# Kernel optimization log

Hardware: AMD Instinct MI355X
Metric: run time of the kernel (lower is better)

The kernel has to match this reference:

```python
import jax, jax.numpy as jnp
import numpy as np

TEMP = 1.75   # temp_schedule(epoch=5, warmup=10): 2.5 - 1.5*0.5
ALPHA = 0.5   # blend_schedule(epoch=5): 0.2 + 0.6*0.5
EPS = 1e-5
HEADS = 2


def _ln(x, g, b):
    mu = x.mean(-1, keepdims=True)
    var = ((x - mu) ** 2).mean(-1, keepdims=True)
    return (x - mu) * jax.lax.rsqrt(var + EPS) * g + b


def _gelu(x):
    return jax.nn.gelu(x, approximate=False)  # torch nn.GELU default = exact erf


def _attn_pool(x, ln_g, ln_b, in_w, in_b, out_w, out_b):
    # x: [N, T, E]; nn.MultiheadAttention self-attention then mean over T
    N, T, E = x.shape
    Dh = E // HEADS
    xn = _ln(x, ln_g, ln_b)
    qkv = xn @ in_w + in_b                      # [N, T, 3E] (in_w stored [E, 3E])
    q, k, v = jnp.split(qkv, 3, axis=-1)
    q = q.reshape(N, T, HEADS, Dh).transpose(0, 2, 1, 3)
    k = k.reshape(N, T, HEADS, Dh).transpose(0, 2, 1, 3)
    v = v.reshape(N, T, HEADS, Dh).transpose(0, 2, 1, 3)
    scores = jnp.einsum('nhqd,nhkd->nhqk', q, k) / jnp.sqrt(jnp.float32(Dh))
    a = jax.nn.softmax(scores, axis=-1)
    o = jnp.einsum('nhqk,nhkd->nhqd', a, v).transpose(0, 2, 1, 3).reshape(N, T, E)
    o = o @ out_w + out_b                       # [N, T, E]
    return o.mean(axis=1)                       # [N, E]


def setup_inputs() -> dict:
    key = jax.random.key(0)
    ks = iter(jax.random.split(key, 40))
    B, L, T, D = 4, 24, 400, 1024
    H = D // 2  # 512
    G = 4       # groups
    s = 0.02
    r = lambda shp: jax.random.normal(next(ks), shp, dtype=jnp.float32) * s
    inp = {
        'x': jax.random.normal(next(ks), (B, L, T, D), dtype=jnp.float32),
        'mlp_alpha': jnp.ones((L,), jnp.float32),
        # shared MLP: LN -> Linear(D,H) -> GELU -> Linear(H,H)
        's_ln_g': jnp.ones((D,), jnp.float32), 's_ln_b': jnp.zeros((D,), jnp.float32),
        's_w1': r((D, H)), 's_b1': jnp.zeros((H,), jnp.float32),
        's_w2': r((H, H)), 's_b2': jnp.zeros((H,), jnp.float32),
        # 4 group MLPs (stacked)
        'g_ln_g': jnp.ones((G, D), jnp.float32), 'g_ln_b': jnp.zeros((G, D), jnp.float32),
        'g_w1': r((G, D, H)), 'g_b1': jnp.zeros((G, H), jnp.float32),
        'g_w2': r((G, H, H)), 'g_b2': jnp.zeros((G, H), jnp.float32),
        # TimeAttentionPool (shared module): LN + MHA(512, 2 heads) + out_proj
        'p_ln_g': jnp.ones((H,), jnp.float32), 'p_ln_b': jnp.zeros((H,), jnp.float32),
        'p_in_w': r((H, 3 * H)), 'p_in_b': jnp.zeros((3 * H,), jnp.float32),
        'p_out_w': r((H, H)), 'p_out_b': jnp.zeros((H,), jnp.float32),
        # router: Linear(512,128) -> GELU -> Linear(128,1) -> sigmoid(/temp)
        'r_w1': r((H, 128)), 'r_b1': jnp.zeros((128,), jnp.float32),
        'r_w2': r((128, 1)), 'r_b2': jnp.zeros((1,), jnp.float32),
        # post norms
        'pn_g': jnp.ones((H,), jnp.float32), 'pn_b': jnp.zeros((H,), jnp.float32),
        'pnf_g': jnp.ones((H,), jnp.float32), 'pnf_b': jnp.zeros((H,), jnp.float32),
        # classifier 512 -> 256 -> 128 -> 2
        'c_w1': r((H, H // 2)), 'c_b1': jnp.zeros((H // 2,), jnp.float32),
        'c_w2': r((H // 2, H // 4)), 'c_b2': jnp.zeros((H // 4,), jnp.float32),
        'c_w3': r((H // 4, 2)), 'c_b3': jnp.zeros((2,), jnp.float32),
    }
    return inp


def reference(x, mlp_alpha, s_ln_g, s_ln_b, s_w1, s_b1, s_w2, s_b2,
              g_ln_g, g_ln_b, g_w1, g_b1, g_w2, g_b2,
              p_ln_g, p_ln_b, p_in_w, p_in_b, p_out_w, p_out_b,
              r_w1, r_b1, r_w2, r_b2, pn_g, pn_b, pnf_g, pnf_b,
              c_w1, c_b1, c_w2, c_b2, c_w3, c_b3):
    B, L, T, D = x.shape
    G = g_w1.shape[0]
    S = L // G  # group_size = 6; expert i uses group i // S
    H = s_w1.shape[1]

    # shared MLP over all experts at once (dropout inactive in eval)
    xs = _ln(x, s_ln_g, s_ln_b)                              # [B,L,T,D]
    shared = _gelu(xs @ s_w1 + s_b1) @ s_w2 + s_b2           # [B,L,T,H]

    # group MLPs: experts i//S -> group; reshape L -> (G, S)
    xg = x.reshape(B, G, S, T, D)
    xgn = _ln(xg, g_ln_g[:, None, None, :], g_ln_b[:, None, None, :])
    hg = _gelu(jnp.einsum('bgstd,gdh->bgsth', xgn, g_w1) + g_b1[None, :, None, None, :])
    grp = jnp.einsum('bgsth,ghk->bgstk', hg, g_w2) + g_b2[None, :, None, None, :]
    grp = grp.reshape(B, L, T, H)

    weighted = shared + mlp_alpha[None, :, None, None] * grp  # [B,L,T,H]

    # attn-pool every expert stream (fold L into batch)
    time_pooled = _attn_pool(weighted.reshape(B * L, T, H),
                             p_ln_g, p_ln_b, p_in_w, p_in_b, p_out_w, p_out_b)
    time_pooled = time_pooled.reshape(B, L, H)               # [B,L,H]

    # router
    rh = _gelu(time_pooled @ r_w1 + r_b1)
    logits_r = (rh @ r_w2 + r_b2)[..., 0]                    # [B,L]
    learned = jax.nn.sigmoid(logits_r / TEMP)
    routing_weights = ALPHA * learned + (1.0 - ALPHA) / L

    # soft fusion over experts
    fusion = (weighted * routing_weights[:, :, None, None]).sum(axis=1)  # [B,T,H]
    fusion = _ln(fusion, pn_g, pn_b).mean(axis=1)            # [B,H]

    shared_mean = shared.mean(axis=1)                        # [B,T,H]
    time_ctx = _attn_pool(shared_mean, p_ln_g, p_ln_b, p_in_w, p_in_b, p_out_w, p_out_b)

    fused_all = _ln(fusion, pnf_g, pnf_b) + _ln(time_ctx, pnf_g, pnf_b)  # [B,H]

    h = _gelu(fused_all @ c_w1 + c_b1)
    h = _gelu(h @ c_w2 + c_b2)
    logits = h @ c_w3 + c_b3                                 # [B,2]
    return logits, routing_weights, fused_all, time_pooled
```

## Files before the change

### kernel.cpp

```cpp
#include <hip/hip_runtime.h>
#include <stdint.h>


typedef float f32x4 __attribute__((ext_vector_type(4)));
typedef short bf16x8 __attribute__((ext_vector_type(8)));

__device__ __forceinline__ float bf2f(unsigned short u) {
  return __uint_as_float(((unsigned int)u) << 16);
}
__device__ __forceinline__ unsigned short f2bf(float f) {
  unsigned int u = __float_as_uint(f);
  u += 0x7fffu + ((u >> 16) & 1u);
  return (unsigned short)(u >> 16);
}
__device__ __forceinline__ float gelu_f(float x) {
  return 0.5f * x * (1.0f + erff(x * 0.70710678118654752440f));
}

typedef __attribute__((address_space(1))) const unsigned int gas_u32;
typedef __attribute__((address_space(3))) unsigned int las_u32;
__device__ __forceinline__ void gload16(const unsigned short* g, unsigned short* l) {
  __builtin_amdgcn_global_load_lds((gas_u32*)g, (las_u32*)l, 16, 0, 0);
}

template <int EPI, int GROUPED>
__global__ __launch_bounds__(256) void gemm_bt(
    const unsigned short* __restrict__ A, const unsigned short* __restrict__ WT,
    const float* __restrict__ bias, unsigned short* __restrict__ Cout,
    const unsigned short* __restrict__ addbuf, const float* __restrict__ alpha_vec,
    unsigned short* __restrict__ vtbuf, int K, int N, int ldout, int Mslice) {
  const int tid = (int)threadIdx.x;
  const int w = tid >> 6, lane = tid & 63, g = lane >> 4, ql = lane & 15;
  const int z = blockIdx.z;
  const int wr = w >> 1, wc = w & 1;

  int bm, bn;
  if (!GROUPED) {
    const int nbm = (int)gridDim.x, nbn = (int)gridDim.y;
    const int nb = nbm * nbn;
    const int lin = (int)blockIdx.x + nbm * (int)blockIdx.y;
    const int q = nb >> 3, r8 = nb & 7;
    const int xcd = lin & 7, c = lin >> 3;
    const int base = (xcd < r8) ? xcd * (q + 1) : r8 * (q + 1) + (xcd - r8) * q;
    const int widx = base + c;
    bm = widx / nbn;
    bn = widx - bm * nbn;
  } else {
    bm = (int)blockIdx.x;
    bn = (int)blockIdx.y;
  }
  const int n0 = bn * 128;

  int rowbase, rows_here;
  const unsigned short* wt = WT;
  const float* bs = bias;
  float alpha = 0.f;
  if (GROUPED) {
    const int l_idx = z % 24;
    const int grp = l_idx / 6;
    rowbase = z * Mslice + bm * 128;
    rows_here = Mslice - bm * 128;
    if (rows_here > 128) rows_here = 128;
    wt = WT + (size_t)grp * (size_t)N * (size_t)K;
    bs = bias + (size_t)grp * (size_t)N;
    if (EPI == 2) alpha = alpha_vec[l_idx];
  } else {
    rowbase = bm * 128;
    rows_here = Mslice - bm * 128;
    if (rows_here > 128) rows_here = 128;
  }

  __shared__ __align__(16) unsigned short sA[2][128 * 32];
  __shared__ __align__(16) unsigned short sB[2][128 * 32];

  f32x4 acc[4][4];
#pragma unroll
  for (int i = 0; i < 4; ++i)
#pragma unroll
    for (int j = 0; j < 4; ++j) acc[i][j] = (f32x4){0.f, 0.f, 0.f, 0.f};

  const int swzg = (lane & 3) ^ ((lane >> 3) & 3);
  const int rA0 = w * 32 + (lane >> 2);
  const int rA1 = rA0 + 16;
  const int rA0c = rA0 < rows_here ? rA0 : rows_here - 1;
  const int rA1c = rA1 < rows_here ? rA1 : rows_here - 1;
  const unsigned short* a0p = A + (size_t)(rowbase + rA0c) * K + swzg * 8;
  const unsigned short* a1p = A + (size_t)(rowbase + rA1c) * K + swzg * 8;
  const unsigned short* b0p = wt + (size_t)(n0 + rA0) * K + swzg * 8;
  const unsigned short* b1p = wt + (size_t)(n0 + rA1) * K + swzg * 8;
  const int ldsw = w * 1024;

  const int aroff = (wr * 64 + ql) * 32 + ((g ^ ((ql >> 1) & 3)) * 8);
  const int broff = (wc * 64 + ql) * 32 + ((g ^ ((ql >> 1) & 3)) * 8);

  const int nsteps = K >> 5;
  gload16(a0p, &sA[0][ldsw]);
  gload16(a1p, &sA[0][ldsw + 512]);
  gload16(b0p, &sB[0][ldsw]);
  gload16(b1p, &sB[0][ldsw + 512]);
  __syncthreads();

  for (int s = 0; s < nsteps; ++s) {
    const int cur = s & 1;
    if (s + 1 < nsteps) {
      const int k0 = (s + 1) << 5;
      const int nxt = cur ^ 1;
      gload16(a0p + k0, &sA[nxt][ldsw]);
      gload16(a1p + k0, &sA[nxt][ldsw + 512]);
      gload16(b0p + k0, &sB[nxt][ldsw]);
      gload16(b1p + k0, &sB[nxt][ldsw + 512]);
    }
    bf16x8 af[4], bfr[4];
#pragma unroll
    for (int mi = 0; mi < 4; ++mi)
      af[mi] = *(const bf16x8*)(&sA[cur][aroff + mi * 512]);
#pragma unroll
    for (int ni = 0; ni < 4; ++ni)
      bfr[ni] = *(const bf16x8*)(&sB[cur][broff + ni * 512]);
#pragma unroll
    for (int mi = 0; mi < 4; ++mi)
#pragma unroll
      for (int ni = 0; ni < 4; ++ni)
        acc[mi][ni] =
            __builtin_amdgcn_mfma_f32_16x16x32_bf16(af[mi], bfr[ni], acc[mi][ni], 0, 0, 0);
    __syncthreads();
  }

#pragma unroll
  for (int mi = 0; mi < 4; ++mi) {
#pragma unroll
    for (int ni = 0; ni < 4; ++ni) {
      const int col = n0 + wc * 64 + ni * 16 + ql;
      const float bb = bs[col];
#pragma unroll
      for (int r = 0; r < 4; ++r) {
        const int rloc = wr * 64 + mi * 16 + 4 * g + r;
        if (rloc >= rows_here) continue;
        const int grow = rowbase + rloc;
        float v = acc[mi][ni][r] + bb;
        if (EPI == 1) v = gelu_f(v);
        if (EPI == 0 || EPI == 1) {
          Cout[(size_t)grow * ldout + col] = f2bf(v);
        } else if (EPI == 2) {
          const float sh = bf2f(addbuf[(size_t)grow * ldout + col]);
          Cout[(size_t)grow * ldout + col] = f2bf(sh + alpha * v);
        } else {
          if (col < 1024) {
            Cout[(size_t)grow * ldout + col] = f2bf(v);
          } else {
            vtbuf[(size_t)grow * 512 + (col - 1024)] = f2bf(v);
          }
        }
      }
    }
  }
}

__global__ void transpose_v(const unsigned short* __restrict__ vbuf,
                            unsigned short* __restrict__ vt) {
  const int p = blockIdx.z;
  const int h = p & 1, nst = p >> 1;
  const int t0 = blockIdx.x * 32, d0 = blockIdx.y * 32;
  __shared__ unsigned short tile[32][33];
  const int tx = threadIdx.x, ty = threadIdx.y;
#pragma unroll
  for (int i = 0; i < 4; ++i) {
    const int t = t0 + ty + i * 8;
    if (t < 400)
      tile[ty + i * 8][tx] = vbuf[((size_t)nst * 400 + t) * 512 + h * 256 + d0 + tx];
  }
  __syncthreads();
  const int t = t0 + tx;
  if (t < 400) {
#pragma unroll
    for (int i = 0; i < 4; ++i)
      vt[((size_t)p * 256 + d0 + ty + i * 8) * 400 + t] = tile[tx][ty + i * 8];
  }
}

__global__ __launch_bounds__(256, 2) void attn_fwd(const unsigned short* __restrict__ qk,
                                                   const unsigned short* __restrict__ vt,
                                                   unsigned short* __restrict__ outb) {
  const int nb = (int)gridDim.x;
  int flat = (int)blockIdx.x;
  flat = (flat & 7) * (nb >> 3) + (flat >> 3);
  const int qt = flat % 7;
  const int h = (flat / 7) & 1;
  const int n = flat / 14;
  const int q0 = qt * 64;

  const int tid = (int)threadIdx.x;
  const int w = tid >> 6, lane = tid & 63, g = lane >> 4, ql = lane & 15;

  __shared__ __align__(16) unsigned short slab[400 * 32];
  __shared__ __align__(16) unsigned short Pc[4][512];
  __shared__ float rs[4][16];

  const int qr = q0 + w * 16 + ql;
  const int qrc = qr < 400 ? qr : 399;
  const unsigned short* qp = qk + ((size_t)n * 400 + qrc) * 1024 + h * 256 + g * 8;
  bf16x8 qf[8];
#pragma unroll
  for (int d0 = 0; d0 < 8; ++d0) qf[d0] = *(const bf16x8*)(qp + d0 * 32);

  f32x4 st[25];
#pragma unroll
  for (int kf = 0; kf < 25; ++kf) st[kf] = (f32x4){0.f, 0.f, 0.f, 0.f};

  const unsigned short* kbase = qk + (size_t)n * 400 * 1024 + 512 + h * 256;
  for (int d0 = 0; d0 < 8; ++d0) {
    bf16x8 stg[7];
#pragma unroll
    for (int c = 0; c < 7; ++c) {
      const int q = tid + c * 256;
      const int r = q >> 2, slot = q & 3;
      if (r < 400)
        stg[c] = *(const bf16x8*)(kbase + (size_t)r * 1024 + d0 * 32 + slot * 8);
    }
    __syncthreads();
#pragma unroll
    for (int c = 0; c < 7; ++c) {
      const int q = tid + c * 256;
      const int r = q >> 2, slot = q & 3;
      if (r < 400) *(bf16x8*)(slab + r * 32 + (slot ^ ((r >> 1) & 3)) * 8) = stg[c];
    }
    __syncthreads();
#pragma unroll
    for (int kf = 0; kf < 25; ++kf) {
      const int r = kf * 16 + ql;
      bf16x8 kfr = *(const bf16x8*)(slab + r * 32 + ((g ^ ((r >> 1) & 3)) * 8));
      st[kf] = __builtin_amdgcn_mfma_f32_16x16x32_bf16(kfr, qf[d0], st[kf], 0, 0, 0);
    }
  }

  const float sc = 0.0625f;
  float m = -3.0e38f;
#pragma unroll
  for (int kf = 0; kf < 25; ++kf)
    m = fmaxf(m, fmaxf(fmaxf(st[kf][0], st[kf][1]), fmaxf(st[kf][2], st[kf][3])));
  m = fmaxf(m, __shfl_xor(m, 16));
  m = fmaxf(m, __shfl_xor(m, 32));
  float sum = 0.f;
  uint2 pp[25];
#pragma unroll
  for (int kf = 0; kf < 25; ++kf) {
    float e0 = expf((st[kf][0] - m) * sc);
    float e1 = expf((st[kf][1] - m) * sc);
    float e2 = expf((st[kf][2] - m) * sc);
    float e3 = expf((st[kf][3] - m) * sc);
    sum += (e0 + e1) + (e2 + e3);
    pp[kf].x = (unsigned int)f2bf(e0) | ((unsigned int)f2bf(e1) << 16);
    pp[kf].y = (unsigned int)f2bf(e2) | ((unsigned int)f2bf(e3) << 16);
  }
  sum += __shfl_xor(sum, 16);
  sum += __shfl_xor(sum, 32);
  if (g == 0) rs[w][ql] = sum;

  f32x4 oacc[16];
#pragma unroll
  for (int nf = 0; nf < 16; ++nf) oacc[nf] = (f32x4){0.f, 0.f, 0.f, 0.f};

  unsigned short* Pw = Pc[w];
  const unsigned short* vbase = vt + (size_t)(n * 2 + h) * 256 * 400;
  for (int kt = 0; kt < 13; ++kt) {
    const int k0 = kt * 32;
    bf16x8 stg[4];
#pragma unroll
    for (int c = 0; c < 4; ++c) {
      const int q = tid + c * 256;
      const int r = q >> 2, slot = q & 3;
      int kc = k0 + slot * 8;
      if (kc >= 400) kc = 0;
      stg[c] = *(const bf16x8*)(vbase + (size_t)r * 400 + kc);
    }
    __syncthreads();
#pragma unroll
    for (int c = 0; c < 4; ++c) {
      const int q = tid + c * 256;
      const int r = q >> 2, slot = q & 3;
      *(bf16x8*)(slab + r * 32 + (slot ^ ((r >> 1) & 3)) * 8) = stg[c];
    }
    {
      const int kf0 = 2 * kt;
      *(uint2*)(Pw + ql * 32 + 4 * g) = pp[kf0];
      uint2 hi = (kf0 + 1 < 25) ? pp[kf0 + 1] : (uint2){0u, 0u};
      *(uint2*)(Pw + ql * 32 + 16 + 4 * g) = hi;
    }
    __syncthreads();
    bf16x8 pa = *(const bf16x8*)(Pw + ql * 32 + g * 8);
#pragma unroll
    for (int nf = 0; nf < 16; ++nf) {
      const int r = nf * 16 + ql;
      bf16x8 vb = *(const bf16x8*)(slab + r * 32 + ((g ^ ((r >> 1) & 3)) * 8));
      oacc[nf] = __builtin_amdgcn_mfma_f32_16x16x32_bf16(pa, vb, oacc[nf], 0, 0, 0);
    }
  }

  const float inv0 = 1.f / rs[w][4 * g + 0];
  const float inv1 = 1.f / rs[w][4 * g + 1];
  const float inv2 = 1.f / rs[w][4 * g + 2];
  const float inv3 = 1.f / rs[w][4 * g + 3];
#pragma unroll
  for (int nf = 0; nf < 16; ++nf) {
#pragma unroll
    for (int r = 0; r < 4; ++r) {
      const int qrow = q0 + w * 16 + 4 * g + r;
      if (qrow < 400) {
        const float invr = (r == 0) ? inv0 : (r == 1) ? inv1 : (r == 2) ? inv2 : inv3;
        outb[((size_t)n * 400 + qrow) * 512 + h * 256 + nf * 16 + ql] =
            f2bf(oacc[nf][r] * invr);
      }
    }
  }
}

template <int TIN, int TOUT>
__global__ void ln_rows(const void* __restrict__ inv, void* __restrict__ outv,
                        const float* __restrict__ gam, const float* __restrict__ bet,
                        int C) {
  const int row = blockIdx.x, t = (int)threadIdx.x;
  float x0, x1, x2, x3;
  if (TIN == 0) {
    float4 v = ((const float4*)inv)[(size_t)row * (C >> 2) + t];
    x0 = v.x; x1 = v.y; x2 = v.z; x3 = v.w;
  } else {
    ushort4 v = ((const ushort4*)inv)[(size_t)row * (C >> 2) + t];
    x0 = bf2f(v.x); x1 = bf2f(v.y); x2 = bf2f(v.z); x3 = bf2f(v.w);
  }
  float s1 = x0 + x1 + x2 + x3;
  float s2 = x0 * x0 + x1 * x1 + x2 * x2 + x3 * x3;
  for (int mlane = 1; mlane < 64; mlane <<= 1) {
    s1 += __shfl_xor(s1, mlane);
    s2 += __shfl_xor(s2, mlane);
  }
  __shared__ float red[8];
  const int nw = blockDim.x >> 6;
  if ((t & 63) == 0) {
    red[t >> 6] = s1;
    red[4 + (t >> 6)] = s2;
  }
  __syncthreads();
  s1 = 0.f; s2 = 0.f;
  for (int i = 0; i < nw; ++i) {
    s1 += red[i];
    s2 += red[4 + i];
  }
  const float mu = s1 / C;
  const float var = s2 / C - mu * mu;
  const float rstd = rsqrtf(var + 1e-5f);
  float y0 = (x0 - mu) * rstd, y1 = (x1 - mu) * rstd, y2 = (x2 - mu) * rstd,
        y3 = (x3 - mu) * rstd;
  if (gam) {
    const int c = t * 4;
    y0 = y0 * gam[c + 0] + bet[c + 0];
    y1 = y1 * gam[c + 1] + bet[c + 1];
    y2 = y2 * gam[c + 2] + bet[c + 2];
    y3 = y3 * gam[c + 3] + bet[c + 3];
  }
  if (TOUT == 0) {
    ushort4 o;
    o.x = f2bf(y0); o.y = f2bf(y1); o.z = f2bf(y2); o.w = f2bf(y3);
    ((ushort4*)outv)[(size_t)row * (C >> 2) + t] = o;
  } else {
    float4 o;
    o.x = y0; o.y = y1; o.z = y2; o.w = y3;
    ((float4*)outv)[(size_t)row * (C >> 2) + t] = o;
  }
}

__global__ void transpose_w(const float* __restrict__ W, const float* __restrict__ scale,
                            unsigned short* __restrict__ WT, int K, int N) {
  __shared__ float tile[32][33];
  const int k0 = blockIdx.x * 32, n0 = blockIdx.y * 32, zg = blockIdx.z;
  const float* Wz = W + (size_t)zg * K * N;
  const float* sz = scale ? scale + (size_t)zg * K : (const float*)0;
  unsigned short* WTz = WT + (size_t)zg * (size_t)K * N;
  const int tx = threadIdx.x, ty = threadIdx.y;
#pragma unroll
  for (int i = 0; i < 4; ++i)
    tile[ty + i * 8][tx] = Wz[(size_t)(k0 + ty + i * 8) * N + n0 + tx];
  __syncthreads();
#pragma unroll
  for (int i = 0; i < 4; ++i) {
    const int nn = n0 + ty + i * 8;
    const int kk = k0 + tx;
    float v = tile[tx][ty + i * 8];
    if (sz) v *= sz[kk];
    WTz[(size_t)nn * K + kk] = f2bf(v);
  }
}

__global__ void transpose_wf(const float* __restrict__ W, float* __restrict__ WT, int K,
                             int N) {
  __shared__ float tile[32][33];
  const int k0 = blockIdx.x * 32, n0 = blockIdx.y * 32;
  const int tx = threadIdx.x, ty = threadIdx.y;
#pragma unroll
  for (int i = 0; i < 4; ++i) {
    const int k = k0 + ty + i * 8;
    if (k < K && n0 + tx < N) tile[ty + i * 8][tx] = W[(size_t)k * N + n0 + tx];
  }
  __syncthreads();
#pragma unroll
  for (int i = 0; i < 4; ++i) {
    const int nn = n0 + ty + i * 8;
    const int kk = k0 + tx;
    if (nn < N && kk < K) WT[(size_t)nn * K + kk] = tile[tx][ty + i * 8];
  }
}

#define BF_KC 16
__global__ void bias_fold_part(const float* __restrict__ W, const float* __restrict__ lb,
                               float* __restrict__ part, int K, int N) {
  const int zg = blockIdx.z;
  const int n = blockIdx.x * 256 + (int)threadIdx.x;
  const int kc = blockIdx.y;
  const int kpc = K / BF_KC;
  const float* Wz = W + (size_t)zg * K * N;
  const float* lbz = lb + (size_t)zg * K;
  float acc = 0.f;
  const int k1 = (kc + 1) * kpc;
  for (int k = kc * kpc; k < k1; ++k) acc += lbz[k] * Wz[(size_t)k * N + n];
  part[((size_t)zg * BF_KC + kc) * N + n] = acc;
}
__global__ void bias_fold_final(const float* __restrict__ part, const float* __restrict__ b,
                                float* __restrict__ beff, int N) {
  const int zg = blockIdx.y;
  const int n = blockIdx.x * 256 + (int)threadIdx.x;
  float acc = b[(size_t)zg * N + n];
#pragma unroll
  for (int c = 0; c < BF_KC; ++c) acc += part[((size_t)zg * BF_KC + c) * N + n];
  beff[(size_t)zg * N + n] = acc;
}

__global__ void mean_l(const unsigned short* __restrict__ sh, float* __restrict__ out) {
  const int i = blockIdx.x * 256 + (int)threadIdx.x;
  if (i >= 4 * 400 * 512 / 4) return;
  const int b = i / (400 * 512 / 4);
  const int rem4 = i - b * (400 * 512 / 4);
  float a0 = 0.f, a1 = 0.f, a2 = 0.f, a3 = 0.f;
  for (int l = 0; l < 24; ++l) {
    ushort4 v = *(const ushort4*)(sh + (size_t)(b * 24 + l) * 204800 + rem4 * 4);
    a0 += bf2f(v.x); a1 += bf2f(v.y); a2 += bf2f(v.z); a3 += bf2f(v.w);
  }
  float4 o;
  o.x = a0 * (1.f / 24.f); o.y = a1 * (1.f / 24.f);
  o.z = a2 * (1.f / 24.f); o.w = a3 * (1.f / 24.f);
  ((float4*)out)[i] = o;
}

template <int TIN>
__global__ void mean_t_part(const void* __restrict__ inv, float* __restrict__ part,
                            int Ns) {
  const int bx = (int)blockIdx.x;
  const int n = bx >> 2, cb = bx & 3;
  const int p = (int)blockIdx.y;
  const int c = cb * 128 + (int)threadIdx.x;
  float acc = 0.f;
  const int t0 = p * 50;
  if (TIN) {
    const unsigned short* in = (const unsigned short*)inv;
    for (int t = t0; t < t0 + 50; ++t) acc += bf2f(in[((size_t)n * 400 + t) * 512 + c]);
  } else {
    const float* in = (const float*)inv;
    for (int t = t0; t < t0 + 50; ++t) acc += in[((size_t)n * 400 + t) * 512 + c];
  }
  part[((size_t)p * Ns + n) * 512 + c] = acc;
}
__global__ void mean_t_fin(const float* __restrict__ part, float* __restrict__ out,
                           int Ns) {
  const int i = (int)blockIdx.x * 256 + (int)threadIdx.x;
  if (i >= Ns * 512) return;
  const int n = i >> 9, c = i & 511;
  float acc = 0.f;
#pragma unroll
  for (int p = 0; p < 8; ++p) acc += part[((size_t)p * Ns + n) * 512 + c];
  out[i] = acc * (1.f / 400.f);
}

__global__ void fuse_ln(const unsigned short* __restrict__ wgt,
                        const float* __restrict__ rw, const float* __restrict__ gam,
                        const float* __restrict__ bet, float* __restrict__ fln) {
  const int row = (int)blockIdx.x;
  const int b = row / 400, tt = row - b * 400;
  const int t = (int)threadIdx.x;
  float a0 = 0.f, a1 = 0.f, a2 = 0.f, a3 = 0.f;
  for (int l = 0; l < 24; ++l) {
    const float wv = rw[b * 24 + l];
    ushort4 v = *(const ushort4*)(wgt + ((size_t)(b * 24 + l) * 400 + tt) * 512 + t * 4);
    a0 += wv * bf2f(v.x); a1 += wv * bf2f(v.y);
    a2 += wv * bf2f(v.z); a3 += wv * bf2f(v.w);
  }
  float s1 = a0 + a1 + a2 + a3;
  float s2 = a0 * a0 + a1 * a1 + a2 * a2 + a3 * a3;
  for (int mlane = 1; mlane < 64; mlane <<= 1) {
    s1 += __shfl_xor(s1, mlane);
    s2 += __shfl_xor(s2, mlane);
  }
  __shared__ float red[4];
  if ((t & 63) == 0) {
    red[t >> 6] = s1;
    red[2 + (t >> 6)] = s2;
  }
  __syncthreads();
  s1 = red[0] + red[1];
  s2 = red[2] + red[3];
  const float mu = s1 * (1.f / 512.f);
  const float var = s2 * (1.f / 512.f) - mu * mu;
  const float rstd = rsqrtf(var + 1e-5f);
  const int c = t * 4;
  float4 o;
  o.x = (a0 - mu) * rstd * gam[c + 0] + bet[c + 0];
  o.y = (a1 - mu) * rstd * gam[c + 1] + bet[c + 1];
  o.z = (a2 - mu) * rstd * gam[c + 2] + bet[c + 2];
  o.w = (a3 - mu) * rstd * gam[c + 3] + bet[c + 3];
  ((float4*)fln)[(size_t)row * 128 + t] = o;
}

__global__ void ln2_add(const float* __restrict__ a, const float* __restrict__ bsrc,
                        const float* __restrict__ gam, const float* __restrict__ bet,
                        float* __restrict__ o1, float* __restrict__ o2) {
  const int row = (int)blockIdx.x;
  const int t = (int)threadIdx.x;
  float4 av = ((const float4*)a)[(size_t)row * 128 + t];
  float4 bv = ((const float4*)bsrc)[(size_t)row * 128 + t];
  float s1a = av.x + av.y + av.z + av.w;
  float s2a = av.x * av.x + av.y * av.y + av.z * av.z + av.w * av.w;
  float s1b = bv.x + bv.y + bv.z + bv.w;
  float s2b = bv.x * bv.x + bv.y * bv.y + bv.z * bv.z + bv.w * bv.w;
  for (int mlane = 1; mlane < 64; mlane <<= 1) {
    s1a += __shfl_xor(s1a, mlane);
    s2a += __shfl_xor(s2a, mlane);
    s1b += __shfl_xor(s1b, mlane);
    s2b += __shfl_xor(s2b, mlane);
  }
  __shared__ float red[8];
  if ((t & 63) == 0) {
    const int wv = t >> 6;
    red[wv] = s1a; red[2 + wv] = s2a; red[4 + wv] = s1b; red[6 + wv] = s2b;
  }
  __syncthreads();
  s1a = red[0] + red[1]; s2a = red[2] + red[3];
  s1b = red[4] + red[5]; s2b = red[6] + red[7];
  const float mua = s1a * (1.f / 512.f);
  const float ra = rsqrtf(s2a * (1.f / 512.f) - mua * mua + 1e-5f);
  const float mub = s1b * (1.f / 512.f);
  const float rb = rsqrtf(s2b * (1.f / 512.f) - mub * mub + 1e-5f);
  const int c = t * 4;
  float4 o;
  o.x = ((av.x - mua) * ra * gam[c + 0] + bet[c + 0]) +
        ((bv.x - mub) * rb * gam[c + 0] + bet[c + 0]);
  o.y = ((av.y - mua) * ra * gam[c + 1] + bet[c + 1]) +
        ((bv.y - mub) * rb * gam[c + 1] + bet[c + 1]);
  o.z = ((av.z - mua) * ra * gam[c + 2] + bet[c + 2]) +
        ((bv.z - mub) * rb * gam[c + 2] + bet[c + 2]);
  o.w = ((av.w - mua) * ra * gam[c + 3] + bet[c + 3]) +
        ((bv.w - mub) * rb * gam[c + 3] + bet[c + 3]);
  ((float4*)o1)[(size_t)row * 128 + t] = o;
  ((float4*)o2)[(size_t)row * 128 + t] = o;
}

template <int WLAYOUT>
__global__ void gemv_wave(const float* __restrict__ A, const float* __restrict__ Wm,
                          const float* __restrict__ b, float* __restrict__ C, int M, int K,
                          int N, int act) {
  const int wid = (int)(blockIdx.x * (blockDim.x >> 6)) + ((int)threadIdx.x >> 6);
  const int lane = (int)threadIdx.x & 63;
  if (wid >= M * N) return;
  const int row = wid / N, col = wid - row * N;
  const float* a = A + (size_t)row * K;
  float acc = 0.f;
  if (WLAYOUT) {
    const float* wt = Wm + (size_t)col * K;
    for (int k = lane; k < K; k += 64) acc += a[k] * wt[k];
  } else {
    for (int k = lane; k < K; k += 64) acc += a[k] * Wm[(size_t)k * N + col];
  }
#pragma unroll
  for (int d = 1; d < 64; d <<= 1) acc += __shfl_xor(acc, d);
  if (lane == 0) {
    acc += b[col];
    if (act) acc = gelu_f(acc);
    C[wid] = acc;
  }
}

__global__ void routing_k(const float* __restrict__ lr, float* __restrict__ o1,
                          float* __restrict__ o2) {
  const int i = (int)threadIdx.x;
  if (i < 96) {
    const float v = 0.5f / (1.f + expf(-lr[i] * (1.f / 1.75f))) + (0.5f / 24.f);
    o1[i] = v;
    o2[i] = v;
  }
}

extern "C" void kernel_launch(void* const* d_in, const int* in_sizes, int n_in,
                              void* d_out, int out_size, void* d_ws, size_t ws_size,
                              hipStream_t stream) {
  const float* x = (const float*)d_in[0];
  const float* mlp_alpha = (const float*)d_in[1];
  const float* s_ln_g = (const float*)d_in[2];
  const float* s_ln_b = (const float*)d_in[3];
  const float* s_w1 = (const float*)d_in[4];
  const float* s_b1 = (const float*)d_in[5];
  const float* s_w2 = (const float*)d_in[6];
  const float* s_b2 = (const float*)d_in[7];
  const float* g_ln_g = (const float*)d_in[8];
  const float* g_ln_b = (const float*)d_in[9];
  const float* g_w1 = (const float*)d_in[10];
  const float* g_b1 = (const float*)d_in[11];
  const float* g_w2 = (const float*)d_in[12];
  const float* g_b2 = (const float*)d_in[13];
  const float* p_ln_g = (const float*)d_in[14];
  const float* p_ln_b = (const float*)d_in[15];
  const float* p_in_w = (const float*)d_in[16];
  const float* p_in_b = (const float*)d_in[17];
  const float* p_out_w = (const float*)d_in[18];
  const float* p_out_b = (const float*)d_in[19];
  const float* r_w1 = (const float*)d_in[20];
  const float* r_b1 = (const float*)d_in[21];
  const float* r_w2 = (const float*)d_in[22];
  const float* r_b2 = (const float*)d_in[23];
  const float* pn_g = (const float*)d_in[24];
  const float* pn_b = (const float*)d_in[25];
  const float* pnf_g = (const float*)d_in[26];
  const float* pnf_b = (const float*)d_in[27];
  const float* c_w1 = (const float*)d_in[28];
  const float* c_b1 = (const float*)d_in[29];
  const float* c_w2 = (const float*)d_in[30];
  const float* c_b2 = (const float*)d_in[31];
  const float* c_w3 = (const float*)d_in[32];
  const float* c_b3 = (const float*)d_in[33];

  float* out = (float*)d_out;
  uint8_t* ws = (uint8_t*)d_ws;

  size_t off = 0;
  auto alloc = [&](size_t bytes) -> size_t {
    size_t o = off;
    off += (bytes + 255) & ~(size_t)255;
    return o;
  };
  const size_t off_xhat = alloc(38400ull * 1024 * 2);
  const size_t off_h = alloc(38400ull * 512 * 2);
  const size_t off_shared = alloc(38400ull * 512 * 2);
  const size_t off_weighted = alloc(38400ull * 512 * 2);
  const size_t off_qk = alloc(38400ull * 1024 * 2);
  const size_t off_pooled = alloc(96ull * 512 * 4);
  const size_t off_rh = alloc(96ull * 128 * 4);
  const size_t off_lr = alloc(96ull * 4);
  const size_t off_rw = alloc(96ull * 4);
  const size_t off_smean = alloc(4ull * 400 * 512 * 4);
  const size_t off_wn2 = alloc(1600ull * 512 * 2);
  const size_t off_qk2 = alloc(1600ull * 1024 * 2);
  const size_t off_vbuf2 = alloc(1600ull * 512 * 2);
  const size_t off_vt2 = alloc(4ull * 2 * 256 * 400 * 2);
  const size_t off_ao2 = alloc(1600ull * 512 * 2);
  const size_t off_pooled2 = alloc(4ull * 512 * 4);
  const size_t off_tctx = alloc(4ull * 512 * 4);
  const size_t off_fln = alloc(4ull * 400 * 512 * 4);
  const size_t off_fvec = alloc(4ull * 512 * 4);
  const size_t off_fall = alloc(4ull * 512 * 4);
  const size_t off_c1 = alloc(4ull * 256 * 4);
  const size_t off_c2 = alloc(4ull * 128 * 4);
  const size_t off_sw1T = alloc(512ull * 1024 * 2);
  const size_t off_sw2T = alloc(512ull * 512 * 2);
  const size_t off_gw1T = alloc(4ull * 512 * 1024 * 2);
  const size_t off_gw2T = alloc(4ull * 512 * 512 * 2);
  const size_t off_pinT = alloc(1536ull * 512 * 2);
  const size_t off_sb1e = alloc(512ull * 4);
  const size_t off_gb1e = alloc(4ull * 512 * 4);
  const size_t off_pinbe = alloc(1536ull * 4);
  const size_t off_bfp_s = alloc((size_t)BF_KC * 512 * 4);
  const size_t off_bfp_g = alloc(4ull * BF_KC * 512 * 4);
  const size_t off_bfp_p = alloc((size_t)BF_KC * 1536 * 4);
  const size_t off_powT = alloc(512ull * 512 * 4);
  const size_t off_rw1T = alloc(128ull * 512 * 4);
  const size_t off_cw1T = alloc(256ull * 512 * 4);
  const size_t off_cw2T = alloc(128ull * 256 * 4);
  const size_t off_mtp = alloc(8ull * 96 * 512 * 4);
  const size_t off_wn = off_xhat;
  const size_t off_vbuf = off_xhat + 38400ull * 512 * 2;
  const size_t off_vt = off_shared;
  const size_t off_ao = off_h;
  if (off > ws_size) return;

  unsigned short* xhat = (unsigned short*)(ws + off_xhat);
  unsigned short* hbuf = (unsigned short*)(ws + off_h);
  unsigned short* sharedb = (unsigned short*)(ws + off_shared);
  unsigned short* weighted = (unsigned short*)(ws + off_weighted);
  unsigned short* qk = (unsigned short*)(ws + off_qk);
  unsigned short* wn = (unsigned short*)(ws + off_wn);
  unsigned short* vbuf = (unsigned short*)(ws + off_vbuf);
  unsigned short* vt = (unsigned short*)(ws + off_vt);
  unsigned short* ao = (unsigned short*)(ws + off_ao);
  float* pooled = (float*)(ws + off_pooled);
  float* rh = (float*)(ws + off_rh);
  float* lr = (float*)(ws + off_lr);
  float* rw = (float*)(ws + off_rw);
  float* smean = (float*)(ws + off_smean);
  unsigned short* wn2 = (unsigned short*)(ws + off_wn2);
  unsigned short* qk2 = (unsigned short*)(ws + off_qk2);
  unsigned short* vbuf2 = (unsigned short*)(ws + off_vbuf2);
  unsigned short* vt2 = (unsigned short*)(ws + off_vt2);
  unsigned short* ao2 = (unsigned short*)(ws + off_ao2);
  float* pooled2 = (float*)(ws + off_pooled2);
  float* tctx = (float*)(ws + off_tctx);
  float* fln = (float*)(ws + off_fln);
  float* fvec = (float*)(ws + off_fvec);
  float* fall = (float*)(ws + off_fall);
  float* c1 = (float*)(ws + off_c1);
  float* c2 = (float*)(ws + off_c2);
  unsigned short* sw1T = (unsigned short*)(ws + off_sw1T);
  unsigned short* sw2T = (unsigned short*)(ws + off_sw2T);
  unsigned short* gw1T = (unsigned short*)(ws + off_gw1T);
  unsigned short* gw2T = (unsigned short*)(ws + off_gw2T);
  unsigned short* pinT = (unsigned short*)(ws + off_pinT);
  float* sb1e = (float*)(ws + off_sb1e);
  float* gb1e = (float*)(ws + off_gb1e);
  float* pinbe = (float*)(ws + off_pinbe);
  float* bfp_s = (float*)(ws + off_bfp_s);
  float* bfp_g = (float*)(ws + off_bfp_g);
  float* bfp_p = (float*)(ws + off_bfp_p);
  float* powT = (float*)(ws + off_powT);
  float* rw1T = (float*)(ws + off_rw1T);
  float* cw1T = (float*)(ws + off_cw1T);
  float* cw2T = (float*)(ws + off_cw2T);
  float* mtp = (float*)(ws + off_mtp);

  transpose_w<<<dim3(32, 16, 1), dim3(32, 8), 0, stream>>>(s_w1, s_ln_g, sw1T, 1024, 512);
  transpose_w<<<dim3(16, 16, 1), dim3(32, 8), 0, stream>>>(s_w2, (const float*)0, sw2T, 512, 512);
  transpose_w<<<dim3(32, 16, 4), dim3(32, 8), 0, stream>>>(g_w1, g_ln_g, gw1T, 1024, 512);
  transpose_w<<<dim3(16, 16, 4), dim3(32, 8), 0, stream>>>(g_w2, (const float*)0, gw2T, 512, 512);
  transpose_w<<<dim3(16, 48, 1), dim3(32, 8), 0, stream>>>(p_in_w, p_ln_g, pinT, 512, 1536);
  transpose_wf<<<dim3(16, 16), dim3(32, 8), 0, stream>>>(p_out_w, powT, 512, 512);
  transpose_wf<<<dim3(16, 4), dim3(32, 8), 0, stream>>>(r_w1, rw1T, 512, 128);
  transpose_wf<<<dim3(16, 8), dim3(32, 8), 0, stream>>>(c_w1, cw1T, 512, 256);
  transpose_wf<<<dim3(8, 4), dim3(32, 8), 0, stream>>>(c_w2, cw2T, 256, 128);
  bias_fold_part<<<dim3(2, BF_KC, 1), 256, 0, stream>>>(s_w1, s_ln_b, bfp_s, 1024, 512);
  bias_fold_final<<<dim3(2, 1), 256, 0, stream>>>(bfp_s, s_b1, sb1e, 512);
  bias_fold_part<<<dim3(2, BF_KC, 4), 256, 0, stream>>>(g_w1, g_ln_b, bfp_g, 1024, 512);
  bias_fold_final<<<dim3(2, 4), 256, 0, stream>>>(bfp_g, g_b1, gb1e, 512);
  bias_fold_part<<<dim3(6, BF_KC, 1), 256, 0, stream>>>(p_in_w, p_ln_b, bfp_p, 512, 1536);
  bias_fold_final<<<dim3(6, 1), 256, 0, stream>>>(bfp_p, p_in_b, pinbe, 1536);

  ln_rows<0, 0><<<38400, 256, 0, stream>>>(x, xhat, (const float*)0, (const float*)0, 1024);

  gemm_bt<1, 0><<<dim3(300, 4, 1), 256, 0, stream>>>(xhat, sw1T, sb1e, hbuf,
      (const unsigned short*)0, (const float*)0, (unsigned short*)0, 1024, 512, 512, 38400);
  gemm_bt<0, 0><<<dim3(300, 4, 1), 256, 0, stream>>>(hbuf, sw2T, s_b2, sharedb,
      (const unsigned short*)0, (const float*)0, (unsigned short*)0, 512, 512, 512, 38400);
  mean_l<<<800, 256, 0, stream>>>(sharedb, smean);

  gemm_bt<1, 1><<<dim3(4, 4, 96), 256, 0, stream>>>(xhat, gw1T, gb1e, hbuf,
      (const unsigned short*)0, (const float*)0, (unsigned short*)0, 1024, 512, 512, 400);
  gemm_bt<2, 1><<<dim3(4, 4, 96), 256, 0, stream>>>(hbuf, gw2T, g_b2, weighted,
      sharedb, mlp_alpha, (unsigned short*)0, 512, 512, 512, 400);

  ln_rows<1, 0><<<38400, 128, 0, stream>>>(weighted, wn, (const float*)0, (const float*)0, 512);
  gemm_bt<3, 0><<<dim3(300, 12, 1), 256, 0, stream>>>(wn, pinT, pinbe, qk,
      (const unsigned short*)0, (const float*)0, vbuf, 512, 1536, 1024, 38400);
  transpose_v<<<dim3(13, 8, 192), dim3(32, 8), 0, stream>>>(vbuf, vt);
  attn_fwd<<<dim3(14 * 96), 256, 0, stream>>>(qk, vt, ao);
  mean_t_part<1><<<dim3(96 * 4, 8), 128, 0, stream>>>(ao, mtp, 96);
  mean_t_fin<<<192, 256, 0, stream>>>(mtp, pooled, 96);
  gemv_wave<1><<<12288, 256, 0, stream>>>(pooled, powT, p_out_b, out + 2152, 96, 512, 512, 0);

  gemv_wave<1><<<3072, 256, 0, stream>>>(out + 2152, rw1T, r_b1, rh, 96, 512, 128, 1);
  gemv_wave<0><<<24, 256, 0, stream>>>(rh, r_w2, r_b2, lr, 96, 128, 1, 0);
  routing_k<<<1, 128, 0, stream>>>(lr, out + 8, rw);

  fuse_ln<<<1600, 128, 0, stream>>>(weighted, rw, pn_g, pn_b, fln);
  mean_t_part<0><<<dim3(4 * 4, 8), 128, 0, stream>>>(fln, mtp, 4);
  mean_t_fin<<<8, 256, 0, stream>>>(mtp, fvec, 4);

  ln_rows<0, 0><<<1600, 128, 0, stream>>>(smean, wn2, (const float*)0, (const float*)0, 512);
  gemm_bt<3, 0><<<dim3(13, 12, 1), 256, 0, stream>>>(wn2, pinT, pinbe, qk2,
      (const unsigned short*)0, (const float*)0, vbuf2, 512, 1536, 1024, 1600);
  transpose_v<<<dim3(13, 8, 8), dim3(32, 8), 0, stream>>>(vbuf2, vt2);
  attn_fwd<<<dim3(14 * 4), 256, 0, stream>>>(qk2, vt2, ao2);
  mean_t_part<1><<<dim3(4 * 4, 8), 128, 0, stream>>>(ao2, mtp, 4);
  mean_t_fin<<<8, 256, 0, stream>>>(mtp, pooled2, 4);
  gemv_wave<1><<<512, 256, 0, stream>>>(pooled2, powT, p_out_b, tctx, 4, 512, 512, 0);

  ln2_add<<<4, 128, 0, stream>>>(fvec, tctx, pnf_g, pnf_b, out + 104, fall);

  gemv_wave<1><<<256, 256, 0, stream>>>(fall, cw1T, c_b1, c1, 4, 512, 256, 1);
  gemv_wave<1><<<128, 256, 0, stream>>>(c1, cw2T, c_b2, c2, 4, 256, 128, 1);
  gemv_wave<0><<<2, 256, 0, stream>>>(c2, c_w3, c_b3, out, 4, 128, 2, 0);
}
```

Measured before the change: 787.7 us.

## Fuse shared and group MLP GEMMs via concatenated weights and linearity

Merges the shared and group first-layer GEMMs into one grouped GEMM with 1024 output columns, the group half scaled by alpha. The second layer becomes a single K=1024 GEMM against concatenated [sw2;gw2] weights with a per-expert folded bias, so the separate shared output buffer and its add-epilogue go away. The mean over L is now taken on the hidden activations before the shared second-layer GEMM, which cuts that GEMM to 1600 rows. The grouped GEMM also gets XCD-aware block swizzling, and the bias-fold split factor is raised. The cost is extra preprocessing kernels, a larger hidden buffer, and a bf16 rounding of the mean where the old code kept it in fp32.

```diff
diff --git a/kernel.cpp b/kernel.cpp
--- a/kernel.cpp
+++ b/kernel.cpp
@@ -27,14 +27,14 @@
 __global__ __launch_bounds__(256) void gemm_bt(
     const unsigned short* __restrict__ A, const unsigned short* __restrict__ WT,
     const float* __restrict__ bias, unsigned short* __restrict__ Cout,
-    const unsigned short* __restrict__ addbuf, const float* __restrict__ alpha_vec,
-    unsigned short* __restrict__ vtbuf, int K, int N, int ldout, int Mslice) {
+    const unsigned short* __restrict__ WT2, const float* __restrict__ bias2,
+    const float* __restrict__ alpha_vec, unsigned short* __restrict__ vtbuf, int K,
+    int N, int ldout, int Mslice) {
   const int tid = (int)threadIdx.x;
   const int w = tid >> 6, lane = tid & 63, g = lane >> 4, ql = lane & 15;
-  const int z = blockIdx.z;
   const int wr = w >> 1, wc = w & 1;
 
-  int bm, bn;
+  int bm, bn, z = 0;
   if (!GROUPED) {
     const int nbm = (int)gridDim.x, nbn = (int)gridDim.y;
     const int nb = nbm * nbn;
@@ -46,12 +46,24 @@
     bm = widx / nbn;
     bn = widx - bm * nbn;
   } else {
-    bm = (int)blockIdx.x;
-    bn = (int)blockIdx.y;
+    const int nbm = (int)gridDim.x, nbn = (int)gridDim.y;
+    const int per_z = nbm * nbn;
+    const int nb = per_z * (int)gridDim.z;
+    const int lin =
+        (int)blockIdx.x + nbm * ((int)blockIdx.y + (int)gridDim.y * (int)blockIdx.z);
+    const int q = nb >> 3, r8 = nb & 7;
+    const int xcd = lin & 7, c = lin >> 3;
+    const int base = (xcd < r8) ? xcd * (q + 1) : r8 * (q + 1) + (xcd - r8) * q;
+    const int widx = base + c;
+    z = widx / per_z;
+    const int rem = widx - z * per_z;
+    bn = rem / nbm;
+    bm = rem - bn * nbm;
   }
   const int n0 = bn * 128;
 
   int rowbase, rows_here;
+  int nw0 = n0;
   const unsigned short* wt = WT;
   const float* bs = bias;
   float alpha = 0.f;
@@ -61,9 +73,20 @@
     rowbase = z * Mslice + bm * 128;
     rows_here = Mslice - bm * 128;
     if (rows_here > 128) rows_here = 128;
-    wt = WT + (size_t)grp * (size_t)N * (size_t)K;
-    bs = bias + (size_t)grp * (size_t)N;
-    if (EPI == 2) alpha = alpha_vec[l_idx];
+    if (EPI == 4) {
+      alpha = alpha_vec[l_idx];
+      if (bn >= 4) {
+        wt = WT2 + (size_t)grp * 512 * (size_t)K;
+        bs = bias2 + (size_t)grp * 512;
+        nw0 = n0 - 512;
+      }
+    } else if (EPI == 5) {
+      wt = WT + (size_t)grp * (size_t)N * (size_t)K;
+      bs = bias2 + (size_t)l_idx * (size_t)N;
+    } else {
+      wt = WT + (size_t)grp * (size_t)N * (size_t)K;
+      bs = bias + (size_t)grp * (size_t)N;
+    }
   } else {
     rowbase = bm * 128;
     rows_here = Mslice - bm * 128;
@@ -86,8 +109,8 @@
   const int rA1c = rA1 < rows_here ? rA1 : rows_here - 1;
   const unsigned short* a0p = A + (size_t)(rowbase + rA0c) * K + swzg * 8;
   const unsigned short* a1p = A + (size_t)(rowbase + rA1c) * K + swzg * 8;
-  const unsigned short* b0p = wt + (size_t)(n0 + rA0) * K + swzg * 8;
-  const unsigned short* b1p = wt + (size_t)(n0 + rA1) * K + swzg * 8;
+  const unsigned short* b0p = wt + (size_t)(nw0 + rA0) * K + swzg * 8;
+  const unsigned short* b1p = wt + (size_t)(nw0 + rA1) * K + swzg * 8;
   const int ldsw = w * 1024;
 
   const int aroff = (wr * 64 + ql) * 32 + ((g ^ ((ql >> 1) & 3)) * 8);
@@ -131,25 +154,24 @@
 #pragma unroll
     for (int ni = 0; ni < 4; ++ni) {
       const int col = n0 + wc * 64 + ni * 16 + ql;
-      const float bb = bs[col];
+      const int colw = (EPI == 4 && bn >= 4) ? (col - 512) : col;
+      const float bb = bs[colw];
 #pragma unroll
       for (int r = 0; r < 4; ++r) {
         const int rloc = wr * 64 + mi * 16 + 4 * g + r;
         if (rloc >= rows_here) continue;
         const int grow = rowbase + rloc;
         float v = acc[mi][ni][r] + bb;
-        if (EPI == 1) v = gelu_f(v);
-        if (EPI == 0 || EPI == 1) {
-          Cout[(size_t)grow * ldout + col] = f2bf(v);
-        } else if (EPI == 2) {
-          const float sh = bf2f(addbuf[(size_t)grow * ldout + col]);
-          Cout[(size_t)grow * ldout + col] = f2bf(sh + alpha * v);
-        } else {
+        if (EPI == 1 || EPI == 4) v = gelu_f(v);
+        if (EPI == 4 && bn >= 4) v *= alpha;
+        if (EPI == 3) {
           if (col < 1024) {
             Cout[(size_t)grow * ldout + col] = f2bf(v);
           } else {
             vtbuf[(size_t)grow * 512 + (col - 1024)] = f2bf(v);
           }
+        } else {
+          Cout[(size_t)grow * ldout + col] = f2bf(v);
         }
       }
     }
@@ -409,7 +431,31 @@
   }
 }
 
-#define BF_KC 16
+__global__ void build_wcomb2(const unsigned short* __restrict__ sw2T,
+                             const unsigned short* __restrict__ gw2T,
+                             unsigned short* __restrict__ wc) {
+  const int q = (int)blockIdx.x * 256 + (int)threadIdx.x;
+  if (q >= 4 * 512 * 256) return;
+  const int grp = q / (512 * 256);
+  const int rem = q - grp * (512 * 256);
+  const int n = rem >> 8, kq = rem & 255;
+  ushort4 v;
+  if (kq < 128) {
+    v = ((const ushort4*)sw2T)[(size_t)n * 128 + kq];
+  } else {
+    v = ((const ushort4*)gw2T)[((size_t)grp * 512 + n) * 128 + (kq - 128)];
+  }
+  ((ushort4*)wc)[q] = v;
+}
+
+__global__ void build_beff2(const float* __restrict__ s_b2, const float* __restrict__ g_b2,
+                            const float* __restrict__ alpha, float* __restrict__ beff2) {
+  const int l = (int)blockIdx.x;
+  const int n = (int)threadIdx.x;
+  beff2[(size_t)l * 512 + n] = s_b2[n] + alpha[l] * g_b2[(size_t)(l / 6) * 512 + n];
+}
+
+#define BF_KC 64
 __global__ void bias_fold_part(const float* __restrict__ W, const float* __restrict__ lb,
                                float* __restrict__ part, int K, int N) {
   const int zg = blockIdx.z;
@@ -433,20 +479,24 @@
   beff[(size_t)zg * N + n] = acc;
 }
 
-__global__ void mean_l(const unsigned short* __restrict__ sh, float* __restrict__ out) {
+__global__ void mean_h(const unsigned short* __restrict__ h,
+                       unsigned short* __restrict__ out) {
   const int i = blockIdx.x * 256 + (int)threadIdx.x;
-  if (i >= 4 * 400 * 512 / 4) return;
-  const int b = i / (400 * 512 / 4);
-  const int rem4 = i - b * (400 * 512 / 4);
+  if (i >= 4 * 400 * 128) return;
+  const int b = i / (400 * 128);
+  const int rem = i - b * (400 * 128);
+  const int t = rem >> 7, c4 = rem & 127;
   float a0 = 0.f, a1 = 0.f, a2 = 0.f, a3 = 0.f;
   for (int l = 0; l < 24; ++l) {
-    ushort4 v = *(const ushort4*)(sh + (size_t)(b * 24 + l) * 204800 + rem4 * 4);
+    ushort4 v = *(const ushort4*)(h + ((size_t)(b * 24 + l) * 400 + t) * 1024 + c4 * 4);
     a0 += bf2f(v.x); a1 += bf2f(v.y); a2 += bf2f(v.z); a3 += bf2f(v.w);
   }
-  float4 o;
-  o.x = a0 * (1.f / 24.f); o.y = a1 * (1.f / 24.f);
-  o.z = a2 * (1.f / 24.f); o.w = a3 * (1.f / 24.f);
-  ((float4*)out)[i] = o;
+  ushort4 o;
+  o.x = f2bf(a0 * (1.f / 24.f));
+  o.y = f2bf(a1 * (1.f / 24.f));
+  o.z = f2bf(a2 * (1.f / 24.f));
+  o.w = f2bf(a3 * (1.f / 24.f));
+  *(ushort4*)(out + ((size_t)(b * 400 + t)) * 512 + c4 * 4) = o;
 }
 
 template <int TIN>
@@ -643,15 +693,15 @@
     return o;
   };
   const size_t off_xhat = alloc(38400ull * 1024 * 2);
-  const size_t off_h = alloc(38400ull * 512 * 2);
-  const size_t off_shared = alloc(38400ull * 512 * 2);
+  const size_t off_h = alloc(38400ull * 1024 * 2);
   const size_t off_weighted = alloc(38400ull * 512 * 2);
   const size_t off_qk = alloc(38400ull * 1024 * 2);
   const size_t off_pooled = alloc(96ull * 512 * 4);
   const size_t off_rh = alloc(96ull * 128 * 4);
   const size_t off_lr = alloc(96ull * 4);
   const size_t off_rw = alloc(96ull * 4);
-  const size_t off_smean = alloc(4ull * 400 * 512 * 4);
+  const size_t off_hmean = alloc(1600ull * 512 * 2);
+  const size_t off_smb = alloc(1600ull * 512 * 2);
   const size_t off_wn2 = alloc(1600ull * 512 * 2);
   const size_t off_qk2 = alloc(1600ull * 1024 * 2);
   const size_t off_vbuf2 = alloc(1600ull * 512 * 2);
@@ -669,9 +719,11 @@
   const size_t off_gw1T = alloc(4ull * 512 * 1024 * 2);
   const size_t off_gw2T = alloc(4ull * 512 * 512 * 2);
   const size_t off_pinT = alloc(1536ull * 512 * 2);
+  const size_t off_wc2 = alloc(4ull * 512 * 1024 * 2);
   const size_t off_sb1e = alloc(512ull * 4);
   const size_t off_gb1e = alloc(4ull * 512 * 4);
   const size_t off_pinbe = alloc(1536ull * 4);
+  const size_t off_beff2 = alloc(24ull * 512 * 4);
   const size_t off_bfp_s = alloc((size_t)BF_KC * 512 * 4);
   const size_t off_bfp_g = alloc(4ull * BF_KC * 512 * 4);
   const size_t off_bfp_p = alloc((size_t)BF_KC * 1536 * 4);
@@ -682,13 +734,12 @@
   const size_t off_mtp = alloc(8ull * 96 * 512 * 4);
   const size_t off_wn = off_xhat;
   const size_t off_vbuf = off_xhat + 38400ull * 512 * 2;
-  const size_t off_vt = off_shared;
   const size_t off_ao = off_h;
+  const size_t off_vt = off_h + 38400ull * 512 * 2;
   if (off > ws_size) return;
 
   unsigned short* xhat = (unsigned short*)(ws + off_xhat);
   unsigned short* hbuf = (unsigned short*)(ws + off_h);
-  unsigned short* sharedb = (unsigned short*)(ws + off_shared);
   unsigned short* weighted = (unsigned short*)(ws + off_weighted);
   unsigned short* qk = (unsigned short*)(ws + off_qk);
   unsigned short* wn = (unsigned short*)(ws + off_wn);
@@ -699,7 +750,8 @@
   float* rh = (float*)(ws + off_rh);
   float* lr = (float*)(ws + off_lr);
   float* rw = (float*)(ws + off_rw);
-  float* smean = (float*)(ws + off_smean);
+  unsigned short* hmean_b = (unsigned short*)(ws + off_hmean);
+  unsigned short* smean_b = (unsigned short*)(ws + off_smb);
   unsigned short* wn2 = (unsigned short*)(ws + off_wn2);
   unsigned short* qk2 = (unsigned short*)(ws + off_qk2);
   unsigned short* vbuf2 = (unsigned short*)(ws + off_vbuf2);
@@ -717,9 +769,11 @@
   unsigned short* gw1T = (unsigned short*)(ws + off_gw1T);
   unsigned short* gw2T = (unsigned short*)(ws + off_gw2T);
   unsigned short* pinT = (unsigned short*)(ws + off_pinT);
+  unsigned short* wcomb2 = (unsigned short*)(ws + off_wc2);
   float* sb1e = (float*)(ws + off_sb1e);
   float* gb1e = (float*)(ws + off_gb1e);
   float* pinbe = (float*)(ws + off_pinbe);
+  float* beff2 = (float*)(ws + off_beff2);
   float* bfp_s = (float*)(ws + off_bfp_s);
   float* bfp_g = (float*)(ws + off_bfp_g);
   float* bfp_p = (float*)(ws + off_bfp_p);
@@ -738,6 +792,8 @@
   transpose_wf<<<dim3(16, 4), dim3(32, 8), 0, stream>>>(r_w1, rw1T, 512, 128);
   transpose_wf<<<dim3(16, 8), dim3(32, 8), 0, stream>>>(c_w1, cw1T, 512, 256);
   transpose_wf<<<dim3(8, 4), dim3(32, 8), 0, stream>>>(c_w2, cw2T, 256, 128);
+  build_wcomb2<<<2048, 256, 0, stream>>>(sw2T, gw2T, wcomb2);
+  build_beff2<<<24, 512, 0, stream>>>(s_b2, g_b2, mlp_alpha, beff2);
   bias_fold_part<<<dim3(2, BF_KC, 1), 256, 0, stream>>>(s_w1, s_ln_b, bfp_s, 1024, 512);
   bias_fold_final<<<dim3(2, 1), 256, 0, stream>>>(bfp_s, s_b1, sb1e, 512);
   bias_fold_part<<<dim3(2, BF_KC, 4), 256, 0, stream>>>(g_w1, g_ln_b, bfp_g, 1024, 512);
@@ -747,20 +803,22 @@
 
   ln_rows<0, 0><<<38400, 256, 0, stream>>>(x, xhat, (const float*)0, (const float*)0, 1024);
 
-  gemm_bt<1, 0><<<dim3(300, 4, 1), 256, 0, stream>>>(xhat, sw1T, sb1e, hbuf,
-      (const unsigned short*)0, (const float*)0, (unsigned short*)0, 1024, 512, 512, 38400);
-  gemm_bt<0, 0><<<dim3(300, 4, 1), 256, 0, stream>>>(hbuf, sw2T, s_b2, sharedb,
-      (const unsigned short*)0, (const float*)0, (unsigned short*)0, 512, 512, 512, 38400);
-  mean_l<<<800, 256, 0, stream>>>(sharedb, smean);
-
-  gemm_bt<1, 1><<<dim3(4, 4, 96), 256, 0, stream>>>(xhat, gw1T, gb1e, hbuf,
-      (const unsigned short*)0, (const float*)0, (unsigned short*)0, 1024, 512, 512, 400);
-  gemm_bt<2, 1><<<dim3(4, 4, 96), 256, 0, stream>>>(hbuf, gw2T, g_b2, weighted,
-      sharedb, mlp_alpha, (unsigned short*)0, 512, 512, 512, 400);
+  gemm_bt<4, 1><<<dim3(4, 8, 96), 256, 0, stream>>>(xhat, sw1T, sb1e, hbuf, gw1T, gb1e,
+      mlp_alpha, (unsigned short*)0, 1024, 1024, 1024, 400);
+
+  gemm_bt<5, 1><<<dim3(4, 4, 96), 256, 0, stream>>>(hbuf, wcomb2, (const float*)0,
+      weighted, (const unsigned short*)0, beff2, (const float*)0, (unsigned short*)0,
+      1024, 512, 512, 400);
+
+  mean_h<<<800, 256, 0, stream>>>(hbuf, hmean_b);
+  gemm_bt<0, 0><<<dim3(13, 4, 1), 256, 0, stream>>>(hmean_b, sw2T, s_b2, smean_b,
+      (const unsigned short*)0, (const float*)0, (const float*)0, (unsigned short*)0,
+      512, 512, 512, 1600);
 
   ln_rows<1, 0><<<38400, 128, 0, stream>>>(weighted, wn, (const float*)0, (const float*)0, 512);
   gemm_bt<3, 0><<<dim3(300, 12, 1), 256, 0, stream>>>(wn, pinT, pinbe, qk,
-      (const unsigned short*)0, (const float*)0, vbuf, 512, 1536, 1024, 38400);
+      (const unsigned short*)0, (const float*)0, (const float*)0, vbuf, 512, 1536, 1024,
+      38400);
   transpose_v<<<dim3(13, 8, 192), dim3(32, 8), 0, stream>>>(vbuf, vt);
   attn_fwd<<<dim3(14 * 96), 256, 0, stream>>>(qk, vt, ao);
   mean_t_part<1><<<dim3(96 * 4, 8), 128, 0, stream>>>(ao, mtp, 96);
@@ -775,9 +833,10 @@
   mean_t_part<0><<<dim3(4 * 4, 8), 128, 0, stream>>>(fln, mtp, 4);
   mean_t_fin<<<8, 256, 0, stream>>>(mtp, fvec, 4);
 
-  ln_rows<0, 0><<<1600, 128, 0, stream>>>(smean, wn2, (const float*)0, (const float*)0, 512);
+  ln_rows<1, 0><<<1600, 128, 0, stream>>>(smean_b, wn2, (const float*)0, (const float*)0, 512);
   gemm_bt<3, 0><<<dim3(13, 12, 1), 256, 0, stream>>>(wn2, pinT, pinbe, qk2,
-      (const unsigned short*)0, (const float*)0, vbuf2, 512, 1536, 1024, 1600);
+      (const unsigned short*)0, (const float*)0, (const float*)0, vbuf2, 512, 1536, 1024,
+      1600);
   transpose_v<<<dim3(13, 8, 8), dim3(32, 8), 0, stream>>>(vbuf2, vt2);
   attn_fwd<<<dim3(14 * 4), 256, 0, stream>>>(qk2, vt2, ao2);
   mean_t_part<1><<<dim3(4 * 4, 8), 128, 0, stream>>>(ao2, mtp, 4);
```

Result: no change. 798.1 us (+1.3%).
